# Performance work log

Measured on AMD Instinct MI355X. Metric: run time of the kernel, lower is better.

The kernel has to match this reference:

```python
import jax, jax.numpy as jnp
import numpy as np

B = 16384          # batch size
S = 7              # grid size (hard-coded in original)
IMG = 448.0        # image size (hard-coded)
CELL = IMG / S     # 64.0 pixels per cell
LAMBDA_COORD = 5.0
LAMBDA_NOOBJ = 0.5


def setup_inputs() -> dict:
    key = jax.random.key(0)
    k1, k2, k3 = jax.random.split(key, 3)
    # predictions: raw head output [B, 30, 7, 7]; keep >= 0.05 so sqrt(w), sqrt(h) are safe
    input_ = jax.random.uniform(k1, (B, 30, S, S), jnp.float32, 0.05, 1.0)
    # targets already channels-last [B, 7, 7, 30]
    target = jax.random.uniform(k2, (B, S, S, 30), jnp.float32, 0.05, 1.0)
    # objectness channel must be exactly 1.0 where an object exists (code tests == 1)
    conf = (jax.random.uniform(k3, (B, S, S)) < 0.25).astype(jnp.float32)
    target = target.at[..., 4].set(conf)
    return {"input_": input_, "target": target}


def _grid_offsets(dtype):
    # flattened [B*49] pixel offsets of each cell's top-left corner
    g = jnp.arange(S, dtype=dtype)
    gx = jnp.broadcast_to(g[None, :], (S, S)).reshape(-1) * CELL  # varies with column
    gy = jnp.broadcast_to(g[:, None], (S, S)).reshape(-1) * CELL  # varies with row
    return jnp.tile(gx, B), jnp.tile(gy, B)


def _decode_box(p, c, gx, gy):
    # p: [N,30]; box at columns c..c+4 -> clamped corner coords in pixels
    cx = p[:, c] * CELL + gx
    cy = p[:, c + 1] * CELL + gy
    w = p[:, c + 2] * IMG
    h = p[:, c + 3] * IMG
    x1 = jnp.clip(cx - w * 0.5, 0.0, IMG)
    y1 = jnp.clip(cy - h * 0.5, 0.0, IMG)
    x2 = jnp.clip(cx + w * 0.5, 0.0, IMG)
    y2 = jnp.clip(cy + h * 0.5, 0.0, IMG)
    return x1, y1, x2, y2


def _iou(a, b):
    ax1, ay1, ax2, ay2 = a
    bx1, by1, bx2, by2 = b
    l = jnp.maximum(ax1, bx1)
    r = jnp.minimum(ax2, bx2)
    t = jnp.maximum(ay1, by1)
    bo = jnp.minimum(ay2, by2)
    m = (l < r) & (t < bo)
    inter = (r - l) * (bo - t)
    union = (ax2 - ax1) * (ay2 - ay1) + (bx2 - bx1) * (by2 - by1)
    denom = union - inter
    return jnp.where(m, inter / jnp.where(m, denom, 1.0), 0.0)


def _yolo_loss(input_, target):
    # [B,30,7,7] -> [B,7,7,30] -> [N,30]
    x = jnp.transpose(input_, (0, 2, 3, 1)).reshape(-1, 30)
    t = target.reshape(-1, 30)
    gx, gy = _grid_offsets(x.dtype)

    iou1 = _iou(_decode_box(x, 0, gx, gy), _decode_box(t, 0, gx, gy))
    iou2 = _iou(_decode_box(x, 5, gx, gy), _decode_box(t, 5, gx, gy))
    mask = iou1 < iou2                      # True -> second predicted box is responsible
    iou = jnp.where(mask, iou2, iou1)

    sel = jnp.where(mask[:, None], x[:, 5:10], x[:, :5])  # responsible box [N,5]
    w = (t[:, 4] == 1.0).astype(x.dtype)                   # hasObj as 0/1 weights

    coord = jnp.sum(w * ((sel[:, 0] - t[:, 0]) ** 2 + (sel[:, 1] - t[:, 1]) ** 2))
    size = jnp.sum(w * ((jnp.sqrt(sel[:, 2]) - jnp.sqrt(t[:, 2])) ** 2
                        + (jnp.sqrt(sel[:, 3]) - jnp.sqrt(t[:, 3])) ** 2))
    conf = jnp.sum(w * (sel[:, 4] - iou) ** 2)
    noobj = jnp.sum((1.0 - w) * sel[:, 4] ** 2)
    cls = jnp.sum(w[:, None] * (x[:, 10:] - t[:, 10:]) ** 2)

    return (LAMBDA_COORD * coord + LAMBDA_COORD * size + conf
            + LAMBDA_NOOBJ * noobj + cls)


def reference(input_, target):
    return _yolo_loss(input_, target)
```

## Files before the change

### kernel.cpp

```cpp
#include <hip/hip_runtime.h>


#define NCH    30
#define CELLS  49
#define TPB    256
#define IMGSZ  448.0f
#define CELLSZ 64.0f

__device__ __forceinline__ float iou_f(float ax1, float ay1, float ax2, float ay2,
                                       float bx1, float by1, float bx2, float by2) {
    float l  = fmaxf(ax1, bx1);
    float r  = fminf(ax2, bx2);
    float t  = fmaxf(ay1, by1);
    float bo = fminf(ay2, by2);
    bool  m  = (l < r) && (t < bo);
    float inter = (r - l) * (bo - t);
    float uni   = (ax2 - ax1) * (ay2 - ay1) + (bx2 - bx1) * (by2 - by1);
    float denom = uni - inter;
    return m ? (inter / denom) : 0.0f;
}

__device__ __forceinline__ void decode_box(float p0, float p1, float p2, float p3,
                                           float gx, float gy,
                                           float& x1, float& y1, float& x2, float& y2) {
    float cx = p0 * CELLSZ + gx;
    float cy = p1 * CELLSZ + gy;
    float w  = p2 * IMGSZ;
    float h  = p3 * IMGSZ;
    x1 = fminf(fmaxf(cx - w * 0.5f, 0.0f), IMGSZ);
    y1 = fminf(fmaxf(cy - h * 0.5f, 0.0f), IMGSZ);
    x2 = fminf(fmaxf(cx + w * 0.5f, 0.0f), IMGSZ);
    y2 = fminf(fmaxf(cy + h * 0.5f, 0.0f), IMGSZ);
}

__device__ __forceinline__ float cell_loss(const float* __restrict__ input,
                                           const float* __restrict__ target,
                                           int n) {
    const int b    = n / CELLS;
    const int cell = n - b * CELLS;

    const float2* __restrict__ tp =
        reinterpret_cast<const float2*>(target) + (long long)n * 15;
    const float* __restrict__ ip = input + (size_t)b * (NCH * CELLS) + cell;

    float2 tv[15];
    float  x[NCH];
    #pragma unroll
    for (int k = 0; k < 15; ++k) tv[k] = tp[k];
    #pragma unroll
    for (int c = 0; c < NCH; ++c) x[c] = ip[c * CELLS];

    float tl[NCH];
    #pragma unroll
    for (int k = 0; k < 15; ++k) { tl[2 * k] = tv[k].x; tl[2 * k + 1] = tv[k].y; }

    const int row  = cell / 7;
    const int col  = cell - row * 7;
    const float gx = (float)col * CELLSZ;
    const float gy = (float)row * CELLSZ;

    float p0x1, p0y1, p0x2, p0y2, p1x1, p1y1, p1x2, p1y2;
    decode_box(x[0], x[1], x[2], x[3], gx, gy, p0x1, p0y1, p0x2, p0y2);
    decode_box(x[5], x[6], x[7], x[8], gx, gy, p1x1, p1y1, p1x2, p1y2);
    float t0x1, t0y1, t0x2, t0y2, t1x1, t1y1, t1x2, t1y2;
    decode_box(tl[0], tl[1], tl[2], tl[3], gx, gy, t0x1, t0y1, t0x2, t0y2);
    decode_box(tl[5], tl[6], tl[7], tl[8], gx, gy, t1x1, t1y1, t1x2, t1y2);

    float iou1 = iou_f(p0x1, p0y1, p0x2, p0y2, t0x1, t0y1, t0x2, t0y2);
    float iou2 = iou_f(p1x1, p1y1, p1x2, p1y2, t1x1, t1y1, t1x2, t1y2);

    bool  mask = iou1 < iou2;
    float iou  = mask ? iou2 : iou1;
    float s0 = mask ? x[5] : x[0];
    float s1 = mask ? x[6] : x[1];
    float s2 = mask ? x[7] : x[2];
    float s3 = mask ? x[8] : x[3];
    float s4 = mask ? x[9] : x[4];

    float w = (tl[4] == 1.0f) ? 1.0f : 0.0f;

    float d0 = s0 - tl[0];
    float d1 = s1 - tl[1];
    float coord = d0 * d0 + d1 * d1;

    float ds2 = sqrtf(s2) - sqrtf(tl[2]);
    float ds3 = sqrtf(s3) - sqrtf(tl[3]);
    float size = ds2 * ds2 + ds3 * ds3;

    float dc = s4 - iou;
    float conf = dc * dc;
    float noobj = s4 * s4;

    float cls = 0.0f;
    #pragma unroll
    for (int c = 10; c < NCH; ++c) {
        float d = x[c] - tl[c];
        cls += d * d;
    }

    return w * (5.0f * (coord + size) + conf + cls) + 0.5f * (1.0f - w) * noobj;
}

template <bool USE_ATOMIC>
__global__ __launch_bounds__(TPB, 4) void yolo_loss_kernel(
        const float* __restrict__ input,
        const float* __restrict__ target,
        float* __restrict__ dst,
        int ncells) {
    __shared__ float red[TPB / 64];

    const int tid = threadIdx.x;
    const int n   = blockIdx.x * TPB + tid;

    float loss = (n < ncells) ? cell_loss(input, target, n) : 0.0f;

    #pragma unroll
    for (int off = 32; off > 0; off >>= 1)
        loss += __shfl_down(loss, off, 64);

    const int wid  = tid >> 6;
    const int lane = tid & 63;
    if (lane == 0) red[wid] = loss;
    __syncthreads();
    if (tid == 0) {
        float s = 0.0f;
        #pragma unroll
        for (int i = 0; i < TPB / 64; ++i) s += red[i];
        if (USE_ATOMIC) atomicAdd(dst, s);
        else            dst[blockIdx.x] = s;
    }
}

__global__ __launch_bounds__(TPB) void reduce_kernel(
        const float* __restrict__ parts, float* __restrict__ out, int n) {
    __shared__ float red[TPB / 64];
    float s = 0.0f;
    for (int i = threadIdx.x; i < n; i += TPB) s += parts[i];
    #pragma unroll
    for (int off = 32; off > 0; off >>= 1)
        s += __shfl_down(s, off, 64);
    const int wid  = threadIdx.x >> 6;
    const int lane = threadIdx.x & 63;
    if (lane == 0) red[wid] = s;
    __syncthreads();
    if (threadIdx.x == 0) {
        float t = 0.0f;
        #pragma unroll
        for (int i = 0; i < TPB / 64; ++i) t += red[i];
        *out = t;
    }
}

extern "C" void kernel_launch(void* const* d_in, const int* in_sizes, int n_in,
                              void* d_out, int out_size, void* d_ws, size_t ws_size,
                              hipStream_t stream) {
    const float* input  = (const float*)d_in[0];
    const float* target = (const float*)d_in[1];
    float* out = (float*)d_out;

    const int ncells = in_sizes[0] / NCH;
    const int blocks = (ncells + TPB - 1) / TPB;

    if (d_ws != nullptr && ws_size >= (size_t)blocks * sizeof(float)) {
        float* parts = (float*)d_ws;
        yolo_loss_kernel<false><<<blocks, TPB, 0, stream>>>(input, target, parts, ncells);
        reduce_kernel<<<1, TPB, 0, stream>>>(parts, out, blocks);
    } else {
        hipMemsetAsync(d_out, 0, sizeof(float), stream);
        yolo_loss_kernel<true><<<blocks, TPB, 0, stream>>>(input, target, out, ncells);
    }
}
```

Measured before the change: 205.9 us.

## Stage input and target tiles into LDS via global_load_lds before compute

Each block now copies its contiguous span of input batches and its target rows into shared memory using 16-byte global_load_lds DMA loads, then each thread reads its strided channels and row from LDS. This replaces uncoalesced per-thread strided global reads, which leave the 120-byte target rows only partly used per access, with fully coalesced bulk copies. The cost is about 77 KB of LDS per block, which caps occupancy at a couple of blocks per CU and drops the previous occupancy hint. There is also a full barrier between loading and compute.

```diff
diff --git a/kernel.cpp b/kernel.cpp
--- a/kernel.cpp
+++ b/kernel.cpp
@@ -6,6 +6,17 @@
 #define TPB    256
 #define IMGSZ  448.0f
 #define CELLSZ 64.0f
+#define BPC    (NCH * CELLS)
+
+#define SMI_FLOATS 11776
+#define SMT_FLOATS (TPB * NCH)
+
+typedef const __attribute__((address_space(1))) unsigned int* gp_t;
+typedef __attribute__((address_space(3))) unsigned int* lp_t;
+
+__device__ __forceinline__ void gload16(const void* g, void* l) {
+    __builtin_amdgcn_global_load_lds((gp_t)g, (lp_t)l, 16, 0, 0);
+}
 
 __device__ __forceinline__ float iou_f(float ax1, float ay1, float ax2, float ay2,
                                        float bx1, float by1, float bx2, float by2) {
@@ -33,93 +44,123 @@
     y2 = fminf(fmaxf(cy + h * 0.5f, 0.0f), IMGSZ);
 }
 
-__device__ __forceinline__ float cell_loss(const float* __restrict__ input,
-                                           const float* __restrict__ target,
-                                           int n) {
-    const int b    = n / CELLS;
-    const int cell = n - b * CELLS;
-
-    const float2* __restrict__ tp =
-        reinterpret_cast<const float2*>(target) + (long long)n * 15;
-    const float* __restrict__ ip = input + (size_t)b * (NCH * CELLS) + cell;
-
-    float2 tv[15];
-    float  x[NCH];
-    #pragma unroll
-    for (int k = 0; k < 15; ++k) tv[k] = tp[k];
-    #pragma unroll
-    for (int c = 0; c < NCH; ++c) x[c] = ip[c * CELLS];
-
-    float tl[NCH];
-    #pragma unroll
-    for (int k = 0; k < 15; ++k) { tl[2 * k] = tv[k].x; tl[2 * k + 1] = tv[k].y; }
-
-    const int row  = cell / 7;
-    const int col  = cell - row * 7;
-    const float gx = (float)col * CELLSZ;
-    const float gy = (float)row * CELLSZ;
-
-    float p0x1, p0y1, p0x2, p0y2, p1x1, p1y1, p1x2, p1y2;
-    decode_box(x[0], x[1], x[2], x[3], gx, gy, p0x1, p0y1, p0x2, p0y2);
-    decode_box(x[5], x[6], x[7], x[8], gx, gy, p1x1, p1y1, p1x2, p1y2);
-    float t0x1, t0y1, t0x2, t0y2, t1x1, t1y1, t1x2, t1y2;
-    decode_box(tl[0], tl[1], tl[2], tl[3], gx, gy, t0x1, t0y1, t0x2, t0y2);
-    decode_box(tl[5], tl[6], tl[7], tl[8], gx, gy, t1x1, t1y1, t1x2, t1y2);
-
-    float iou1 = iou_f(p0x1, p0y1, p0x2, p0y2, t0x1, t0y1, t0x2, t0y2);
-    float iou2 = iou_f(p1x1, p1y1, p1x2, p1y2, t1x1, t1y1, t1x2, t1y2);
-
-    bool  mask = iou1 < iou2;
-    float iou  = mask ? iou2 : iou1;
-    float s0 = mask ? x[5] : x[0];
-    float s1 = mask ? x[6] : x[1];
-    float s2 = mask ? x[7] : x[2];
-    float s3 = mask ? x[8] : x[3];
-    float s4 = mask ? x[9] : x[4];
-
-    float w = (tl[4] == 1.0f) ? 1.0f : 0.0f;
-
-    float d0 = s0 - tl[0];
-    float d1 = s1 - tl[1];
-    float coord = d0 * d0 + d1 * d1;
-
-    float ds2 = sqrtf(s2) - sqrtf(tl[2]);
-    float ds3 = sqrtf(s3) - sqrtf(tl[3]);
-    float size = ds2 * ds2 + ds3 * ds3;
-
-    float dc = s4 - iou;
-    float conf = dc * dc;
-    float noobj = s4 * s4;
-
-    float cls = 0.0f;
-    #pragma unroll
-    for (int c = 10; c < NCH; ++c) {
-        float d = x[c] - tl[c];
-        cls += d * d;
-    }
-
-    return w * (5.0f * (coord + size) + conf + cls) + 0.5f * (1.0f - w) * noobj;
-}
-
 template <bool USE_ATOMIC>
-__global__ __launch_bounds__(TPB, 4) void yolo_loss_kernel(
+__global__ __launch_bounds__(TPB) void yolo_loss_kernel(
         const float* __restrict__ input,
         const float* __restrict__ target,
         float* __restrict__ dst,
         int ncells) {
     __shared__ float red[TPB / 64];
-
-    const int tid = threadIdx.x;
-    const int n   = blockIdx.x * TPB + tid;
-
-    float loss = (n < ncells) ? cell_loss(input, target, n) : 0.0f;
+    __shared__ __align__(16) float smi[SMI_FLOATS];
+    __shared__ __align__(16) float smt[SMT_FLOATS];
+
+    const int tid  = threadIdx.x;
+    const int n0   = blockIdx.x * TPB;
+    const int rows = min(TPB, ncells - n0);
+    const int wid  = tid >> 6;
+    const int lane = tid & 63;
+
+    const int b_lo = n0 / CELLS;
+    const int b_hi = (n0 + rows - 1) / CELLS;
+    const int b0   = b_lo & ~1;
+    const size_t in_base = (size_t)b0 * BPC;
+    const int span_fl = (b_hi - b0 + 1) * BPC;
+    const int n16i    = span_fl >> 2;
+
+    const size_t tg_base = (size_t)n0 * NCH;
+    const int tfl  = rows * NCH;
+    const int n16t = tfl >> 2;
+
+    const int ct = (n16t + 63) >> 6;
+    const int ci = (n16i + 63) >> 6;
+    for (int c = wid; c < ct; c += TPB / 64) {
+        int i  = c * 64 + lane;
+        int ig = min(i, n16t - 1);
+        gload16(target + tg_base + (size_t)ig * 4, (char*)smt + (size_t)i * 16);
+    }
+    for (int c = wid; c < ci; c += TPB / 64) {
+        int i  = c * 64 + lane;
+        int ig = min(i, n16i - 1);
+        gload16(input + in_base + (size_t)ig * 4, (char*)smi + (size_t)i * 16);
+    }
+    if ((span_fl & 3) && tid < (span_fl & 3))
+        smi[(n16i << 2) + tid] = input[in_base + (n16i << 2) + tid];
+    if ((tfl & 3) && tid < (tfl & 3))
+        smt[(n16t << 2) + tid] = target[tg_base + (n16t << 2) + tid];
+
+    __syncthreads();
+
+    float loss = 0.0f;
+    if (tid < rows) {
+        const int n    = n0 + tid;
+        const int b    = n / CELLS;
+        const int cell = n - b * CELLS;
+
+        const float* ip = smi + (b - b0) * BPC + cell;
+        float x[NCH];
+        #pragma unroll
+        for (int c = 0; c < NCH; ++c) x[c] = ip[c * CELLS];
+
+        const float* trow = smt + tid * NCH;
+        float tl[NCH];
+        #pragma unroll
+        for (int k = 0; k < NCH / 2; ++k) {
+            float2 v = *reinterpret_cast<const float2*>(trow + 2 * k);
+            tl[2 * k]     = v.x;
+            tl[2 * k + 1] = v.y;
+        }
+
+        const int row  = cell / 7;
+        const int col  = cell - row * 7;
+        const float gx = (float)col * CELLSZ;
+        const float gy = (float)row * CELLSZ;
+
+        float p0x1, p0y1, p0x2, p0y2, p1x1, p1y1, p1x2, p1y2;
+        decode_box(x[0], x[1], x[2], x[3], gx, gy, p0x1, p0y1, p0x2, p0y2);
+        decode_box(x[5], x[6], x[7], x[8], gx, gy, p1x1, p1y1, p1x2, p1y2);
+        float t0x1, t0y1, t0x2, t0y2, t1x1, t1y1, t1x2, t1y2;
+        decode_box(tl[0], tl[1], tl[2], tl[3], gx, gy, t0x1, t0y1, t0x2, t0y2);
+        decode_box(tl[5], tl[6], tl[7], tl[8], gx, gy, t1x1, t1y1, t1x2, t1y2);
+
+        float iou1 = iou_f(p0x1, p0y1, p0x2, p0y2, t0x1, t0y1, t0x2, t0y2);
+        float iou2 = iou_f(p1x1, p1y1, p1x2, p1y2, t1x1, t1y1, t1x2, t1y2);
+
+        bool  mask = iou1 < iou2;
+        float iou  = mask ? iou2 : iou1;
+        float s0 = mask ? x[5] : x[0];
+        float s1 = mask ? x[6] : x[1];
+        float s2 = mask ? x[7] : x[2];
+        float s3 = mask ? x[8] : x[3];
+        float s4 = mask ? x[9] : x[4];
+
+        float w = (tl[4] == 1.0f) ? 1.0f : 0.0f;
+
+        float d0 = s0 - tl[0];
+        float d1 = s1 - tl[1];
+        float coord = d0 * d0 + d1 * d1;
+
+        float ds2 = sqrtf(s2) - sqrtf(tl[2]);
+        float ds3 = sqrtf(s3) - sqrtf(tl[3]);
+        float size = ds2 * ds2 + ds3 * ds3;
+
+        float dc = s4 - iou;
+        float conf = dc * dc;
+        float noobj = s4 * s4;
+
+        float cls = 0.0f;
+        #pragma unroll
+        for (int c = 10; c < NCH; ++c) {
+            float d = x[c] - tl[c];
+            cls += d * d;
+        }
+
+        loss = w * (5.0f * (coord + size) + conf + cls) + 0.5f * (1.0f - w) * noobj;
+    }
 
     #pragma unroll
     for (int off = 32; off > 0; off >>= 1)
         loss += __shfl_down(loss, off, 64);
 
-    const int wid  = tid >> 6;
-    const int lane = tid & 63;
     if (lane == 0) red[wid] = loss;
     __syncthreads();
     if (tid == 0) {
```

After: 205.2 us. No clear change (-0.4%).
